# Optimization experiments

Hardware: AMD Instinct MI355X
Metric: run time of the kernel (lower is better)

## Reference

```python
import jax, jax.numpy as jnp
import numpy as np

N = 50000      # nodes
E = 800000     # edges (avg degree 16)
D_IN = 64
H = 128        # capacity
LAT = 64       # latent_dim
LN_EPS = 1e-5


def setup_inputs() -> dict:
    key = jax.random.key(0)
    ks = jax.random.split(key, 16)
    inp = {}
    inp["x"] = jax.random.normal(ks[0], (N, D_IN), dtype=jnp.float32)
    inp["edge_index"] = jax.random.randint(ks[1], (2, E), 0, N)
    dims = [(D_IN, H), (H, H), (H, LAT)]
    ki = 2
    for t in ("m", "v"):  # mu tower / logvar tower
        for i, (di, do) in enumerate(dims):
            s = 1.0 / np.sqrt(di)
            inp[f"{t}Wl{i}"] = jax.random.normal(ks[ki], (do, di), jnp.float32) * s; ki += 1
            inp[f"{t}bl{i}"] = jnp.zeros((do,), jnp.float32)
            inp[f"{t}Wr{i}"] = jax.random.normal(ks[ki], (do, di), jnp.float32) * s; ki += 1
            if i < 2:  # LayerNorm on hidden layers only
                inp[f"{t}g{i}"] = jnp.ones((do,), jnp.float32)
                inp[f"{t}b{i}"] = jnp.zeros((do,), jnp.float32)
    return inp


def _ln(h, g, b):
    m = h.mean(-1, keepdims=True)
    v = h.var(-1, keepdims=True)
    return (h - m) * jax.lax.rsqrt(v + LN_EPS) * g + b


def _sage(h, src, dst, inv_deg, Wl, bl, Wr):
    # mean neighbor aggregation: scatter-add messages h[src] into dst, divide by degree
    agg = jax.ops.segment_sum(h[src], dst, num_segments=N) * inv_deg  # [N, d_in]
    # PyG SAGEConv: lin_l(agg) [with bias] + lin_r(h_root) [no bias]
    return agg @ Wl.T + bl + h @ Wr.T


def _tower(x, src, dst, inv_deg, layers):
    h = x
    L = len(layers)
    for i, lay in enumerate(layers):
        h = _sage(h, src, dst, inv_deg, lay[0], lay[1], lay[2])
        if i < L - 1:
            h = jax.nn.relu(_ln(h, lay[3], lay[4]))
    return h


def reference(x, edge_index,
              mWl0, mbl0, mWr0, mg0, mb0,
              mWl1, mbl1, mWr1, mg1, mb1,
              mWl2, mbl2, mWr2,
              vWl0, vbl0, vWr0, vg0, vb0,
              vWl1, vbl1, vWr1, vg1, vb1,
              vWl2, vbl2, vWr2):
    src, dst = edge_index[0], edge_index[1]
    deg = jax.ops.segment_sum(jnp.ones((E,), x.dtype), dst, num_segments=N)
    inv_deg = (1.0 / jnp.maximum(deg, 1.0))[:, None]
    mu_layers = [(mWl0, mbl0, mWr0, mg0, mb0),
                 (mWl1, mbl1, mWr1, mg1, mb1),
                 (mWl2, mbl2, mWr2)]
    lv_layers = [(vWl0, vbl0, vWr0, vg0, vb0),
                 (vWl1, vbl1, vWr1, vg1, vb1),
                 (vWl2, vbl2, vWr2)]
    mu = _tower(x, src, dst, inv_deg, mu_layers)
    lv = _tower(x, src, dst, inv_deg, lv_layers)
    return mu, lv
```

## Files before the change

### kernel.cpp

```cpp
#include <hip/hip_runtime.h>

#define NN 50000
#define NE 800000
#define MPAD 50048
#define NBK 196
#define FB 98
#define CH4 2048
#define EB4 200000
#define STAGE_CAP 6144

typedef __attribute__((ext_vector_type(8))) short short8;
typedef __attribute__((ext_vector_type(4))) float f32x4;

__device__ __forceinline__ ushort f2b(float f) {
    uint u = __builtin_bit_cast(uint, f);
    uint r = (u + 0x7fffu + ((u >> 16) & 1u)) >> 16;
    return (ushort)r;
}
__device__ __forceinline__ uint pk2(float a, float b) {
    return (uint)f2b(a) | ((uint)f2b(b) << 16);
}
__device__ __forceinline__ float blo(uint u) { return __builtin_bit_cast(float, u << 16); }
__device__ __forceinline__ float bhi(uint u) { return __builtin_bit_cast(float, u & 0xffff0000u); }


__global__ __launch_bounds__(256) void k_f1(const int* __restrict__ dst, int* __restrict__ bhist) {
    __shared__ int h[NBK];
    for (int i = threadIdx.x; i < NBK; i += 256) h[i] = 0;
    __syncthreads();
    int i1 = min((int)(blockIdx.x + 1) * CH4, EB4);
    for (int i = blockIdx.x * CH4 + threadIdx.x; i < i1; i += 256) {
        int4 d = ((const int4*)dst)[i];
        atomicAdd(&h[d.x >> 8], 1);
        atomicAdd(&h[d.y >> 8], 1);
        atomicAdd(&h[d.z >> 8], 1);
        atomicAdd(&h[d.w >> 8], 1);
    }
    __syncthreads();
    for (int i = threadIdx.x; i < NBK; i += 256) bhist[blockIdx.x * NBK + i] = h[i];
}

__global__ __launch_bounds__(256) void k_fscan(const int* __restrict__ bhist,
                                               int* __restrict__ pairRel,
                                               int* __restrict__ bbase) {
    __shared__ int tot[256];
    int b = threadIdx.x;
    int run = 0;
    if (b < NBK) {
        for (int blk = 0; blk < FB; ++blk) {
            int v = bhist[blk * NBK + b];
            pairRel[blk * NBK + b] = run;
            run += v;
        }
    }
    tot[b] = (b < NBK) ? run : 0;
    __syncthreads();
    for (int off = 1; off < 256; off <<= 1) {
        int t = (b >= off) ? tot[b - off] : 0;
        __syncthreads();
        tot[b] += t;
        __syncthreads();
    }
    if (b < NBK) bbase[b] = tot[b] - run;
    if (b == NBK - 1) bbase[NBK] = tot[b];
}

__global__ __launch_bounds__(256) void k_f2(const int* __restrict__ src, const int* __restrict__ dst,
                                            const int* __restrict__ pairRel,
                                            const int* __restrict__ bbase, int2* __restrict__ pairs) {
    __shared__ int cur[NBK];
    for (int i = threadIdx.x; i < NBK; i += 256)
        cur[i] = bbase[i] + pairRel[blockIdx.x * NBK + i];
    __syncthreads();
    int i1 = min((int)(blockIdx.x + 1) * CH4, EB4);
    for (int i = blockIdx.x * CH4 + threadIdx.x; i < i1; i += 256) {
        int4 s = ((const int4*)src)[i];
        int4 d = ((const int4*)dst)[i];
        int p0 = atomicAdd(&cur[d.x >> 8], 1);
        int p1 = atomicAdd(&cur[d.y >> 8], 1);
        int p2 = atomicAdd(&cur[d.z >> 8], 1);
        int p3 = atomicAdd(&cur[d.w >> 8], 1);
        pairs[p0] = (int2){s.x, d.x};
        pairs[p1] = (int2){s.y, d.y};
        pairs[p2] = (int2){s.z, d.z};
        pairs[p3] = (int2){s.w, d.w};
    }
}

__global__ __launch_bounds__(256) void k_f3(const int2* __restrict__ pairs,
                                            const int* __restrict__ bbase,
                                            int* __restrict__ row_start,
                                            float* __restrict__ inv_deg,
                                            int* __restrict__ col) {
    __shared__ int ndeg[256];
    __shared__ int noff[256];
    __shared__ int stage[STAGE_CAP];
    int b = blockIdx.x;
    int base = bbase[b], end = bbase[b + 1];
    int nbase = b << 8;
    int t = threadIdx.x;
    ndeg[t] = 0;
    __syncthreads();
    for (int p = base + t; p < end; p += 256) atomicAdd(&ndeg[pairs[p].y - nbase], 1);
    __syncthreads();
    int d = ndeg[t];
    noff[t] = d;
    __syncthreads();
    for (int off = 1; off < 256; off <<= 1) {
        int v = (t >= off) ? noff[t - off] : 0;
        __syncthreads();
        noff[t] += v;
        __syncthreads();
    }
    int excl = noff[t] - d;
    int node = nbase + t;
    if (node < NN) {
        row_start[node] = base + excl;
        inv_deg[node] = 1.0f / (float)(d > 1 ? d : 1);
    }
    if (b == 0 && t == 0) row_start[NN] = NE;
    __syncthreads();
    noff[t] = excl;
    __syncthreads();
    int cnt = end - base;
    for (int p = base + t; p < end; p += 256) {
        int2 pr = pairs[p];
        int pos = atomicAdd(&noff[pr.y - nbase], 1);
        if (pos < STAGE_CAP) stage[pos] = pr.x;
        else col[base + pos] = pr.x;
    }
    __syncthreads();
    int lim = cnt < STAGE_CAP ? cnt : STAGE_CAP;
    for (int i = t; i < lim; i += 256) col[base + i] = stage[i];
}


__global__ void k_xcvt(const float* __restrict__ x, ushort* __restrict__ xb, int n2) {
    int i = blockIdx.x * blockDim.x + threadIdx.x;
    if (i < n2) {
        float2 v = *(const float2*)(x + (size_t)i * 2);
        *(uint*)(xb + (size_t)i * 2) = pk2(v.x, v.y);
    }
}

struct W2Args {
    const float* srcA[8];
    const float* srcB[8];
    ushort* dst[8];
};

__global__ void k_wcvt(W2Args a) {
    const int offT[8]   = {0, 16384, 49152, 57344, 65536, 81920, 114688, 122880};
    const int splitT[8] = {64, 128, 128, 0, 64, 128, 128, 0};
    const int logKKT[8] = {7, 8, 7, 7, 7, 8, 7, 7};
    const int ntT[8]    = {8, 8, 4, 4, 8, 8, 4, 4};
    int idx = blockIdx.x * blockDim.x + threadIdx.x;
    if (idx >= 131072) return;
    int L = 0;
#pragma unroll
    for (int i = 1; i < 8; ++i) if (idx >= offT[i]) L = i;
    int j = idx - offT[L];
    int lk = logKKT[L];
    int KK = 1 << lk;
    int n = j >> lk;
    int c = j & (KK - 1);
    int split = splitT[L];
    float v = (c < split) ? a.srcA[L][n * split + c]
                          : a.srcB[L][n * (KK - split) + (c - split)];
    int ks = c >> 5, kseg = (c >> 3) & 3, jj = c & 7;
    int nt = n >> 4, r15 = n & 15;
    int lane = (kseg << 4) | r15;
    int foff = ((ks * ntT[L] + nt) << 9) + (lane << 3) + jj;
    a.dst[L][foff] = f2b(v);
}


__device__ __forceinline__ void acc8(float* a, uint4 u) {
    a[0] += blo(u.x); a[1] += bhi(u.x);
    a[2] += blo(u.y); a[3] += bhi(u.y);
    a[4] += blo(u.z); a[5] += bhi(u.z);
    a[6] += blo(u.w); a[7] += bhi(u.w);
}

template <int D, int NSLICE>
__global__ __launch_bounds__(256) void k_aggs(
    const ushort* __restrict__ h,
    const int* __restrict__ row_start, const int* __restrict__ col,
    const float* __restrict__ inv_deg, ushort* __restrict__ o) {
    int slice = blockIdx.x % NSLICE;
    int chunk = blockIdx.x / NSLICE;
    int node = chunk * 64 + (threadIdx.x >> 2);
    int li = threadIdx.x & 3;
    if (node >= NN) return;
    int s = row_start[node], e = row_start[node + 1];
    float sc = inv_deg[node];
    const ushort* hb = h + (size_t)slice * 32 + (size_t)li * 8;
    float a[8] = {0, 0, 0, 0, 0, 0, 0, 0};
    int p = s;
    for (; p + 7 < e; p += 8) {
        int c0 = col[p], c1 = col[p + 1], c2 = col[p + 2], c3 = col[p + 3];
        int c4 = col[p + 4], c5 = col[p + 5], c6 = col[p + 6], c7 = col[p + 7];
        uint4 u0 = *(const uint4*)(hb + (size_t)c0 * D);
        uint4 u1 = *(const uint4*)(hb + (size_t)c1 * D);
        uint4 u2 = *(const uint4*)(hb + (size_t)c2 * D);
        uint4 u3 = *(const uint4*)(hb + (size_t)c3 * D);
        uint4 u4 = *(const uint4*)(hb + (size_t)c4 * D);
        uint4 u5 = *(const uint4*)(hb + (size_t)c5 * D);
        uint4 u6 = *(const uint4*)(hb + (size_t)c6 * D);
        uint4 u7 = *(const uint4*)(hb + (size_t)c7 * D);
        acc8(a, u0); acc8(a, u1); acc8(a, u2); acc8(a, u3);
        acc8(a, u4); acc8(a, u5); acc8(a, u6); acc8(a, u7);
    }
    for (; p < e; ++p) acc8(a, *(const uint4*)(hb + (size_t)col[p] * D));
    uint4 r;
    r.x = pk2(a[0] * sc, a[1] * sc);
    r.y = pk2(a[2] * sc, a[3] * sc);
    r.z = pk2(a[4] * sc, a[5] * sc);
    r.w = pk2(a[6] * sc, a[7] * sc);
    *(uint4*)(o + (size_t)node * D + slice * 32 + li * 8) = r;
}


struct GArgs {
    const ushort *A1, *A2, *Wm, *Wv;
    const float *blm, *blv, *gm, *gv, *bbm, *bbv;
    void* out;
};

template <int KH, int NOUT, bool DO_LN, bool DUAL, int ASTR, int AOFFM, int OSTR, int OOFFM>
__global__ __launch_bounds__(256, 2) void k_gemm(GArgs a) {
    constexpr int NT = NOUT / 16;
    constexpr int NK = KH / 16;
    constexpr int TW = DUAL ? 2 : 1;
    constexpr int WCH = NOUT * KH * 4 / 16;
    __shared__ uint4 wlds[TW * WCH];

    int tid = threadIdx.x;
    int lane = tid & 63, wid = tid >> 6;
    int tow = DUAL ? 0 : blockIdx.y;
    int aoff = tow * AOFFM;

    {
        const uint4* w0 = (const uint4*)(tow ? a.Wv : a.Wm);
        for (int i = tid; i < WCH; i += 256) wlds[i] = w0[i];
        if (DUAL) {
            const uint4* w1 = (const uint4*)a.Wv;
            for (int i = tid; i < WCH; i += 256) wlds[WCH + i] = w1[i];
        }
    }

    int r15 = lane & 15, kseg = lane >> 4;
    int m0 = blockIdx.x * 128 + wid * 32;
    size_t ar0 = (size_t)(m0 + r15);
    size_t ar1 = (size_t)(m0 + 16 + r15);

    short8 af[2][NK];
#pragma unroll
    for (int ks = 0; ks < NK; ++ks) {
        int kc = ks * 32 + kseg * 8;
        af[0][ks] = (kc < KH) ? *(const short8*)(a.A1 + ar0 * ASTR + aoff + kc)
                              : *(const short8*)(a.A2 + ar0 * ASTR + aoff + (kc - KH));
        af[1][ks] = (kc < KH) ? *(const short8*)(a.A1 + ar1 * ASTR + aoff + kc)
                              : *(const short8*)(a.A2 + ar1 * ASTR + aoff + (kc - KH));
    }
    __syncthreads();

    f32x4 acc[TW][2][NT];
#pragma unroll
    for (int tt = 0; tt < TW; ++tt)
#pragma unroll
        for (int t = 0; t < 2; ++t)
#pragma unroll
            for (int nt = 0; nt < NT; ++nt) acc[tt][t][nt] = (f32x4){0.f, 0.f, 0.f, 0.f};

#pragma unroll
    for (int ks = 0; ks < NK; ++ks) {
#pragma unroll
        for (int nt = 0; nt < NT; ++nt) {
#pragma unroll
            for (int tt = 0; tt < TW; ++tt) {
                short8 w = *(const short8*)&wlds[tt * WCH + (ks * NT + nt) * 64 + lane];
                acc[tt][0][nt] = __builtin_amdgcn_mfma_f32_16x16x32_bf16(af[0][ks], w, acc[tt][0][nt], 0, 0, 0);
                acc[tt][1][nt] = __builtin_amdgcn_mfma_f32_16x16x32_bf16(af[1][ks], w, acc[tt][1][nt], 0, 0, 0);
            }
        }
    }

#pragma unroll
    for (int tt = 0; tt < TW; ++tt) {
        int tsel = DUAL ? tt : tow;
        int ooff = tsel * OOFFM;
        const float* bl = tsel ? a.blv : a.blm;
#pragma unroll
        for (int nt = 0; nt < NT; ++nt) {
            float bb = bl[nt * 16 + r15];
#pragma unroll
            for (int t = 0; t < 2; ++t)
#pragma unroll
                for (int r = 0; r < 4; ++r) acc[tt][t][nt][r] += bb;
        }
        if (DO_LN) {
            const float* g = tsel ? a.gv : a.gm;
            const float* b = tsel ? a.bbv : a.bbm;
#pragma unroll
            for (int t = 0; t < 2; ++t) {
                float s[4] = {0, 0, 0, 0}, q[4] = {0, 0, 0, 0};
#pragma unroll
                for (int nt = 0; nt < NT; ++nt)
#pragma unroll
                    for (int r = 0; r < 4; ++r) { float v = acc[tt][t][nt][r]; s[r] += v; q[r] += v * v; }
#pragma unroll
                for (int off = 1; off < 16; off <<= 1)
#pragma unroll
                    for (int r = 0; r < 4; ++r) { s[r] += __shfl_xor(s[r], off); q[r] += __shfl_xor(q[r], off); }
                float mean[4], rstd[4];
#pragma unroll
                for (int r = 0; r < 4; ++r) {
                    mean[r] = s[r] * (1.0f / NOUT);
                    float var = q[r] * (1.0f / NOUT) - mean[r] * mean[r];
                    rstd[r] = rsqrtf(var + 1e-5f);
                }
                ushort* out = (ushort*)a.out;
#pragma unroll
                for (int nt = 0; nt < NT; ++nt) {
                    int n = nt * 16 + r15;
                    float gg = g[n], bb = b[n];
#pragma unroll
                    for (int r = 0; r < 4; ++r) {
                        int row = m0 + t * 16 + kseg * 4 + r;
                        if (row < NN) {
                            float y = fmaxf((acc[tt][t][nt][r] - mean[r]) * rstd[r] * gg + bb, 0.0f);
                            out[(size_t)row * OSTR + ooff + n] = f2b(y);
                        }
                    }
                }
            }
        } else {
            float* out = (float*)a.out;
#pragma unroll
            for (int t = 0; t < 2; ++t)
#pragma unroll
                for (int nt = 0; nt < NT; ++nt) {
                    int n = nt * 16 + r15;
#pragma unroll
                    for (int r = 0; r < 4; ++r) {
                        int row = m0 + t * 16 + kseg * 4 + r;
                        if (row < NN) out[(size_t)row * OSTR + ooff + n] = acc[tt][t][nt][r];
                    }
                }
        }
    }
}


struct G2Args {
    const ushort *A, *Wm, *Wv, *a2;
    const float *blm, *blv;
    void *outm, *outv;
};

template <bool FINAL>
__global__ __launch_bounds__(256, 2) void k_gemm2(G2Args a) {
    constexpr int NT = 4, NK = 4;
    constexpr int WCH = 1024;
    __shared__ uint4 wlds[WCH];

    int tid = threadIdx.x;
    int lane = tid & 63, wid = tid >> 6;
    int tow = blockIdx.y;
    {
        const uint4* w0 = (const uint4*)(tow ? a.Wv : a.Wm);
        for (int i = tid; i < WCH; i += 256) wlds[i] = w0[i];
    }
    int r15 = lane & 15, kseg = lane >> 4;
    int m0 = blockIdx.x * 128 + wid * 32;
    size_t ar0 = (size_t)(m0 + r15);
    size_t ar1 = (size_t)(m0 + 16 + r15);
    int aoff = tow * 128;

    short8 af[2][NK];
#pragma unroll
    for (int ks = 0; ks < NK; ++ks) {
        int kc = ks * 32 + kseg * 8;
        af[0][ks] = *(const short8*)(a.A + ar0 * 256 + aoff + kc);
        af[1][ks] = *(const short8*)(a.A + ar1 * 256 + aoff + kc);
    }
    __syncthreads();

    f32x4 acc[2][NT];
#pragma unroll
    for (int t = 0; t < 2; ++t)
#pragma unroll
        for (int nt = 0; nt < NT; ++nt) acc[t][nt] = (f32x4){0.f, 0.f, 0.f, 0.f};

#pragma unroll
    for (int ks = 0; ks < NK; ++ks) {
#pragma unroll
        for (int nt = 0; nt < NT; ++nt) {
            short8 w = *(const short8*)&wlds[(ks * NT + nt) * 64 + lane];
            acc[0][nt] = __builtin_amdgcn_mfma_f32_16x16x32_bf16(af[0][ks], w, acc[0][nt], 0, 0, 0);
            acc[1][nt] = __builtin_amdgcn_mfma_f32_16x16x32_bf16(af[1][ks], w, acc[1][nt], 0, 0, 0);
        }
    }

    if (FINAL) {
        const float* bl = tow ? a.blv : a.blm;
        float* out = (float*)(tow ? a.outv : a.outm);
#pragma unroll
        for (int t = 0; t < 2; ++t)
#pragma unroll
            for (int nt = 0; nt < NT; ++nt) {
                int n = nt * 16 + r15;
                float bb = bl[n];
#pragma unroll
                for (int r = 0; r < 4; ++r) {
                    int row = m0 + t * 16 + kseg * 4 + r;
                    if (row < NN) {
                        float av = blo((uint)a.a2[(size_t)row * 128 + tow * 64 + n]);
                        out[(size_t)row * 64 + n] = acc[t][nt][r] + bb + av;
                    }
                }
            }
    } else {
        ushort* out = (ushort*)a.outm;
#pragma unroll
        for (int t = 0; t < 2; ++t)
#pragma unroll
            for (int nt = 0; nt < NT; ++nt) {
                int n = nt * 16 + r15;
#pragma unroll
                for (int r = 0; r < 4; ++r) {
                    int row = m0 + t * 16 + kseg * 4 + r;
                    if (row < NN) out[(size_t)row * 128 + tow * 64 + n] = f2b(acc[t][nt][r]);
                }
            }
    }
}


extern "C" void kernel_launch(void* const* d_in, const int* in_sizes, int n_in,
                              void* d_out, int out_size, void* d_ws, size_t ws_size,
                              hipStream_t stream) {
    const float* x = (const float*)d_in[0];
    const int* ei = (const int*)d_in[1];
    const int* esrc = ei;
    const int* edst = ei + NE;

    const float* mWl0 = (const float*)d_in[2];
    const float* mbl0 = (const float*)d_in[3];
    const float* mWr0 = (const float*)d_in[4];
    const float* mg0  = (const float*)d_in[5];
    const float* mb0  = (const float*)d_in[6];
    const float* mWl1 = (const float*)d_in[7];
    const float* mbl1 = (const float*)d_in[8];
    const float* mWr1 = (const float*)d_in[9];
    const float* mg1  = (const float*)d_in[10];
    const float* mb1  = (const float*)d_in[11];
    const float* mWl2 = (const float*)d_in[12];
    const float* mbl2 = (const float*)d_in[13];
    const float* mWr2 = (const float*)d_in[14];
    const float* vWl0 = (const float*)d_in[15];
    const float* vbl0 = (const float*)d_in[16];
    const float* vWr0 = (const float*)d_in[17];
    const float* vg0  = (const float*)d_in[18];
    const float* vb0  = (const float*)d_in[19];
    const float* vWl1 = (const float*)d_in[20];
    const float* vbl1 = (const float*)d_in[21];
    const float* vWr1 = (const float*)d_in[22];
    const float* vg1  = (const float*)d_in[23];
    const float* vb1  = (const float*)d_in[24];
    const float* vWl2 = (const float*)d_in[25];
    const float* vbl2 = (const float*)d_in[26];
    const float* vWr2 = (const float*)d_in[27];

    char* p = (char*)d_ws;
    auto alloc = [&](size_t bytes) {
        void* r = (void*)p;
        p += (bytes + 255) & ~(size_t)255;
        return r;
    };
    int* bhist     = (int*)alloc((size_t)FB * NBK * 4);
    int* pairRel   = (int*)alloc((size_t)FB * NBK * 4);
    int* bbase     = (int*)alloc((size_t)(NBK + 1) * 4);
    int* row_start = (int*)alloc((size_t)(NN + 1) * 4);
    float* inv_deg = (float*)alloc((size_t)NN * 4);
    int* col       = (int*)alloc((size_t)NE * 4);
    int2* pairs    = (int2*)alloc((size_t)NE * 8);
    ushort* agg0   = (ushort*)pairs;
    ushort* x_bf   = (ushort*)alloc((size_t)MPAD * 64 * 2);
    ushort* h1p    = (ushort*)alloc((size_t)MPAD * 256 * 2);
    ushort* h2p    = (ushort*)alloc((size_t)MPAD * 256 * 2);
    ushort* aggp   = (ushort*)alloc((size_t)MPAD * 256 * 2);
    ushort* p2     = aggp;
    ushort* a2     = aggp + (size_t)MPAD * 128;
    ushort* wc0    = (ushort*)alloc((size_t)128 * 128 * 2);
    ushort* wc1    = (ushort*)alloc((size_t)128 * 256 * 2);
    ushort* wc2    = (ushort*)alloc((size_t)64 * 128 * 2);
    ushort* wc3    = (ushort*)alloc((size_t)128 * 128 * 2);
    ushort* wc4    = (ushort*)alloc((size_t)128 * 256 * 2);
    ushort* wc5    = (ushort*)alloc((size_t)64 * 128 * 2);
    ushort* wc6    = (ushort*)alloc((size_t)64 * 128 * 2);
    ushort* wc7    = (ushort*)alloc((size_t)64 * 128 * 2);

    float* out_mu = (float*)d_out;
    float* out_lv = (float*)d_out + (size_t)NN * 64;

    k_xcvt<<<(NN * 64 / 2 + 255) / 256, 256, 0, stream>>>(x, x_bf, NN * 64 / 2);
    W2Args wa;
    wa.srcA[0] = mWl0; wa.srcB[0] = mWr0; wa.dst[0] = wc0;
    wa.srcA[1] = mWl1; wa.srcB[1] = mWr1; wa.dst[1] = wc1;
    wa.srcA[2] = mWl2; wa.srcB[2] = nullptr; wa.dst[2] = wc2;
    wa.srcA[3] = nullptr; wa.srcB[3] = mWr2; wa.dst[3] = wc6;
    wa.srcA[4] = vWl0; wa.srcB[4] = vWr0; wa.dst[4] = wc3;
    wa.srcA[5] = vWl1; wa.srcB[5] = vWr1; wa.dst[5] = wc4;
    wa.srcA[6] = vWl2; wa.srcB[6] = nullptr; wa.dst[6] = wc5;
    wa.srcA[7] = nullptr; wa.srcB[7] = vWr2; wa.dst[7] = wc7;
    k_wcvt<<<512, 256, 0, stream>>>(wa);

    k_f1<<<FB, 256, 0, stream>>>(edst, bhist);
    k_fscan<<<1, 256, 0, stream>>>(bhist, pairRel, bbase);
    k_f2<<<FB, 256, 0, stream>>>(esrc, edst, pairRel, bbase, pairs);
    k_f3<<<196, 256, 0, stream>>>(pairs, bbase, row_start, inv_deg, col);

    const int CHK = (NN + 63) / 64;
    const int gM = MPAD / 128;

    k_aggs<64, 2><<<2 * CHK, 256, 0, stream>>>(x_bf, row_start, col, inv_deg, agg0);
    {
        GArgs ga = {agg0, x_bf, wc0, wc3, mbl0, vbl0, mg0, vg0, mb0, vb0, h1p};
        k_gemm<64, 128, true, true, 64, 0, 256, 128><<<dim3(gM, 1), 256, 0, stream>>>(ga);
    }
    k_aggs<256, 8><<<8 * CHK, 256, 0, stream>>>(h1p, row_start, col, inv_deg, aggp);
    {
        GArgs ga = {aggp, h1p, wc1, wc4, mbl1, vbl1, mg1, vg1, mb1, vb1, h2p};
        k_gemm<128, 128, true, false, 256, 128, 256, 128><<<dim3(gM, 2), 256, 0, stream>>>(ga);
    }
    {
        G2Args g2 = {h2p, wc2, wc5, nullptr, nullptr, nullptr, p2, nullptr};
        k_gemm2<false><<<dim3(gM, 2), 256, 0, stream>>>(g2);
    }
    k_aggs<128, 4><<<4 * CHK, 256, 0, stream>>>(p2, row_start, col, inv_deg, a2);
    {
        G2Args g2 = {h2p, wc6, wc7, a2, mbl2, vbl2, out_mu, out_lv};
        k_gemm2<true><<<dim3(gM, 2), 256, 0, stream>>>(g2);
    }
}
```

Before: 392.7 us.

## Merge prep kernels and restructure gather aggregation with whole-row lane mapping

Fuses the x conversion, weight conversion and destination histogram into a single prep launch to cut launch overhead. Rewrites neighbour aggregation so all lanes for one node cover the full feature row in one block instead of slicing features across blocks. It also unrolls the edge loop by 16 and adds nontemporal loads and stores for column indices, pairs and outputs. The intent is fewer launches and more memory-level parallelism per gather, at the cost of more register pressure. For D=64 each lane now does narrower 8-byte loads.

After: 375.5 us. 1.05x faster.

```diff
diff --git a/kernel.cpp b/kernel.cpp
--- a/kernel.cpp
+++ b/kernel.cpp
@@ -11,6 +11,9 @@
 
 typedef __attribute__((ext_vector_type(8))) short short8;
 typedef __attribute__((ext_vector_type(4))) float f32x4;
+typedef uint __attribute__((ext_vector_type(4))) uintx4;
+typedef uint __attribute__((ext_vector_type(2))) uintx2;
+typedef int __attribute__((ext_vector_type(2))) intx2;
 
 __device__ __forceinline__ ushort f2b(float f) {
     uint u = __builtin_bit_cast(uint, f);
@@ -23,22 +26,80 @@
 __device__ __forceinline__ float blo(uint u) { return __builtin_bit_cast(float, u << 16); }
 __device__ __forceinline__ float bhi(uint u) { return __builtin_bit_cast(float, u & 0xffff0000u); }
 
-
-__global__ __launch_bounds__(256) void k_f1(const int* __restrict__ dst, int* __restrict__ bhist) {
+__device__ __forceinline__ void acc8(float* a, uintx4 u) {
+    a[0] += blo(u[0]); a[1] += bhi(u[0]);
+    a[2] += blo(u[1]); a[3] += bhi(u[1]);
+    a[4] += blo(u[2]); a[5] += bhi(u[2]);
+    a[6] += blo(u[3]); a[7] += bhi(u[3]);
+}
+__device__ __forceinline__ void acc4(float* a, uintx2 u) {
+    a[0] += blo(u[0]); a[1] += bhi(u[0]);
+    a[2] += blo(u[1]); a[3] += bhi(u[1]);
+}
+
+
+struct W2Args {
+    const float* srcA[8];
+    const float* srcB[8];
+    ushort* dst[8];
+};
+
+
+struct PrepArgs {
+    const float* x; ushort* xb;
+    W2Args w;
+    const int* edst; int* bhist;
+};
+
+__global__ __launch_bounds__(256) void k_prep(PrepArgs a) {
     __shared__ int h[NBK];
-    for (int i = threadIdx.x; i < NBK; i += 256) h[i] = 0;
-    __syncthreads();
-    int i1 = min((int)(blockIdx.x + 1) * CH4, EB4);
-    for (int i = blockIdx.x * CH4 + threadIdx.x; i < i1; i += 256) {
-        int4 d = ((const int4*)dst)[i];
-        atomicAdd(&h[d.x >> 8], 1);
-        atomicAdd(&h[d.y >> 8], 1);
-        atomicAdd(&h[d.z >> 8], 1);
-        atomicAdd(&h[d.w >> 8], 1);
-    }
-    __syncthreads();
-    for (int i = threadIdx.x; i < NBK; i += 256) bhist[blockIdx.x * NBK + i] = h[i];
-}
+    int b = blockIdx.x;
+    int t = threadIdx.x;
+    if (b < FB) {
+        for (int i = t; i < NBK; i += 256) h[i] = 0;
+        __syncthreads();
+        int i1 = min((b + 1) * CH4, EB4);
+        for (int i = b * CH4 + t; i < i1; i += 256) {
+            int4 d = ((const int4*)a.edst)[i];
+            atomicAdd(&h[d.x >> 8], 1);
+            atomicAdd(&h[d.y >> 8], 1);
+            atomicAdd(&h[d.z >> 8], 1);
+            atomicAdd(&h[d.w >> 8], 1);
+        }
+        __syncthreads();
+        for (int i = t; i < NBK; i += 256) a.bhist[b * NBK + i] = h[i];
+    } else if (b < FB + 512) {
+        const int offT[8]   = {0, 16384, 49152, 57344, 65536, 81920, 114688, 122880};
+        const int splitT[8] = {64, 128, 128, 0, 64, 128, 128, 0};
+        const int logKKT[8] = {7, 8, 7, 7, 7, 8, 7, 7};
+        const int ntT[8]    = {8, 8, 4, 4, 8, 8, 4, 4};
+        int idx = (b - FB) * 256 + t;
+        if (idx >= 131072) return;
+        int L = 0;
+#pragma unroll
+        for (int i = 1; i < 8; ++i) if (idx >= offT[i]) L = i;
+        int j = idx - offT[L];
+        int lk = logKKT[L];
+        int KK = 1 << lk;
+        int n = j >> lk;
+        int c = j & (KK - 1);
+        int split = splitT[L];
+        float v = (c < split) ? a.w.srcA[L][n * split + c]
+                              : a.w.srcB[L][n * (KK - split) + (c - split)];
+        int ks = c >> 5, kseg = (c >> 3) & 3, jj = c & 7;
+        int nt = n >> 4, r15 = n & 15;
+        int lane = (kseg << 4) | r15;
+        int foff = ((ks * ntT[L] + nt) << 9) + (lane << 3) + jj;
+        a.w.dst[L][foff] = f2b(v);
+    } else {
+        int i = (b - FB - 512) * 256 + t;
+        if (i < NN * 32) {
+            float2 v = *(const float2*)(a.x + (size_t)i * 2);
+            *(uint*)(a.xb + (size_t)i * 2) = pk2(v.x, v.y);
+        }
+    }
+}
+
 
 __global__ __launch_bounds__(256) void k_fscan(const int* __restrict__ bhist,
                                                int* __restrict__ pairRel,
@@ -67,7 +128,7 @@
 
 __global__ __launch_bounds__(256) void k_f2(const int* __restrict__ src, const int* __restrict__ dst,
                                             const int* __restrict__ pairRel,
-                                            const int* __restrict__ bbase, int2* __restrict__ pairs) {
+                                            const int* __restrict__ bbase, intx2* __restrict__ pairs) {
     __shared__ int cur[NBK];
     for (int i = threadIdx.x; i < NBK; i += 256)
         cur[i] = bbase[i] + pairRel[blockIdx.x * NBK + i];
@@ -80,14 +141,14 @@
         int p1 = atomicAdd(&cur[d.y >> 8], 1);
         int p2 = atomicAdd(&cur[d.z >> 8], 1);
         int p3 = atomicAdd(&cur[d.w >> 8], 1);
-        pairs[p0] = (int2){s.x, d.x};
-        pairs[p1] = (int2){s.y, d.y};
-        pairs[p2] = (int2){s.z, d.z};
-        pairs[p3] = (int2){s.w, d.w};
-    }
-}
-
-__global__ __launch_bounds__(256) void k_f3(const int2* __restrict__ pairs,
+        __builtin_nontemporal_store((intx2){s.x, d.x}, &pairs[p0]);
+        __builtin_nontemporal_store((intx2){s.y, d.y}, &pairs[p1]);
+        __builtin_nontemporal_store((intx2){s.z, d.z}, &pairs[p2]);
+        __builtin_nontemporal_store((intx2){s.w, d.w}, &pairs[p3]);
+    }
+}
+
+__global__ __launch_bounds__(256) void k_f3(const intx2* __restrict__ pairs,
                                             const int* __restrict__ bbase,
                                             int* __restrict__ row_start,
                                             float* __restrict__ inv_deg,
@@ -101,7 +162,10 @@
     int t = threadIdx.x;
     ndeg[t] = 0;
     __syncthreads();
-    for (int p = base + t; p < end; p += 256) atomicAdd(&ndeg[pairs[p].y - nbase], 1);
+    for (int p = base + t; p < end; p += 256) {
+        intx2 pr = pairs[p];
+        atomicAdd(&ndeg[pr[1] - nbase], 1);
+    }
     __syncthreads();
     int d = ndeg[t];
     noff[t] = d;
@@ -124,10 +188,10 @@
     __syncthreads();
     int cnt = end - base;
     for (int p = base + t; p < end; p += 256) {
-        int2 pr = pairs[p];
-        int pos = atomicAdd(&noff[pr.y - nbase], 1);
-        if (pos < STAGE_CAP) stage[pos] = pr.x;
-        else col[base + pos] = pr.x;
+        intx2 pr = pairs[p];
+        int pos = atomicAdd(&noff[pr[1] - nbase], 1);
+        if (pos < STAGE_CAP) stage[pos] = pr[0];
+        else col[base + pos] = pr[0];
     }
     __syncthreads();
     int lim = cnt < STAGE_CAP ? cnt : STAGE_CAP;
@@ -135,89 +199,67 @@
 }
 
 
-__global__ void k_xcvt(const float* __restrict__ x, ushort* __restrict__ xb, int n2) {
-    int i = blockIdx.x * blockDim.x + threadIdx.x;
-    if (i < n2) {
-        float2 v = *(const float2*)(x + (size_t)i * 2);
-        *(uint*)(xb + (size_t)i * 2) = pk2(v.x, v.y);
-    }
-}
-
-struct W2Args {
-    const float* srcA[8];
-    const float* srcB[8];
-    ushort* dst[8];
-};
-
-__global__ void k_wcvt(W2Args a) {
-    const int offT[8]   = {0, 16384, 49152, 57344, 65536, 81920, 114688, 122880};
-    const int splitT[8] = {64, 128, 128, 0, 64, 128, 128, 0};
-    const int logKKT[8] = {7, 8, 7, 7, 7, 8, 7, 7};
-    const int ntT[8]    = {8, 8, 4, 4, 8, 8, 4, 4};
-    int idx = blockIdx.x * blockDim.x + threadIdx.x;
-    if (idx >= 131072) return;
-    int L = 0;
-#pragma unroll
-    for (int i = 1; i < 8; ++i) if (idx >= offT[i]) L = i;
-    int j = idx - offT[L];
-    int lk = logKKT[L];
-    int KK = 1 << lk;
-    int n = j >> lk;
-    int c = j & (KK - 1);
-    int split = splitT[L];
-    float v = (c < split) ? a.srcA[L][n * split + c]
-                          : a.srcB[L][n * (KK - split) + (c - split)];
-    int ks = c >> 5, kseg = (c >> 3) & 3, jj = c & 7;
-    int nt = n >> 4, r15 = n & 15;
-    int lane = (kseg << 4) | r15;
-    int foff = ((ks * ntT[L] + nt) << 9) + (lane << 3) + jj;
-    a.dst[L][foff] = f2b(v);
-}
-
-
-__device__ __forceinline__ void acc8(float* a, uint4 u) {
-    a[0] += blo(u.x); a[1] += bhi(u.x);
-    a[2] += blo(u.y); a[3] += bhi(u.y);
-    a[4] += blo(u.z); a[5] += bhi(u.z);
-    a[6] += blo(u.w); a[7] += bhi(u.w);
-}
-
-template <int D, int NSLICE>
-__global__ __launch_bounds__(256) void k_aggs(
+template <int D>
+__global__ __launch_bounds__(256) void k_agg(
     const ushort* __restrict__ h,
     const int* __restrict__ row_start, const int* __restrict__ col,
     const float* __restrict__ inv_deg, ushort* __restrict__ o) {
-    int slice = blockIdx.x % NSLICE;
-    int chunk = blockIdx.x / NSLICE;
-    int node = chunk * 64 + (threadIdx.x >> 2);
-    int li = threadIdx.x & 3;
+    constexpr int LPN = (D == 256) ? 32 : 16;
+    int gid = blockIdx.x * 256 + threadIdx.x;
+    int node = gid / LPN;
+    int li = gid & (LPN - 1);
     if (node >= NN) return;
     int s = row_start[node], e = row_start[node + 1];
     float sc = inv_deg[node];
-    const ushort* hb = h + (size_t)slice * 32 + (size_t)li * 8;
-    float a[8] = {0, 0, 0, 0, 0, 0, 0, 0};
-    int p = s;
-    for (; p + 7 < e; p += 8) {
-        int c0 = col[p], c1 = col[p + 1], c2 = col[p + 2], c3 = col[p + 3];
-        int c4 = col[p + 4], c5 = col[p + 5], c6 = col[p + 6], c7 = col[p + 7];
-        uint4 u0 = *(const uint4*)(hb + (size_t)c0 * D);
-        uint4 u1 = *(const uint4*)(hb + (size_t)c1 * D);
-        uint4 u2 = *(const uint4*)(hb + (size_t)c2 * D);
-        uint4 u3 = *(const uint4*)(hb + (size_t)c3 * D);
-        uint4 u4 = *(const uint4*)(hb + (size_t)c4 * D);
-        uint4 u5 = *(const uint4*)(hb + (size_t)c5 * D);
-        uint4 u6 = *(const uint4*)(hb + (size_t)c6 * D);
-        uint4 u7 = *(const uint4*)(hb + (size_t)c7 * D);
-        acc8(a, u0); acc8(a, u1); acc8(a, u2); acc8(a, u3);
-        acc8(a, u4); acc8(a, u5); acc8(a, u6); acc8(a, u7);
-    }
-    for (; p < e; ++p) acc8(a, *(const uint4*)(hb + (size_t)col[p] * D));
-    uint4 r;
-    r.x = pk2(a[0] * sc, a[1] * sc);
-    r.y = pk2(a[2] * sc, a[3] * sc);
-    r.z = pk2(a[4] * sc, a[5] * sc);
-    r.w = pk2(a[6] * sc, a[7] * sc);
-    *(uint4*)(o + (size_t)node * D + slice * 32 + li * 8) = r;
+    if (D == 64) {
+        const ushort* hb = h + li * 4;
+        float a[4] = {0, 0, 0, 0};
+        int p = s;
+        for (; p + 15 < e; p += 16) {
+            int cc[16];
+#pragma unroll
+            for (int j = 0; j < 16; ++j) cc[j] = __builtin_nontemporal_load(col + p + j);
+#pragma unroll
+            for (int j = 0; j < 16; ++j) acc4(a, *(const uintx2*)(hb + (size_t)cc[j] * 64));
+        }
+        for (; p + 3 < e; p += 4) {
+            int cc[4];
+#pragma unroll
+            for (int j = 0; j < 4; ++j) cc[j] = __builtin_nontemporal_load(col + p + j);
+#pragma unroll
+            for (int j = 0; j < 4; ++j) acc4(a, *(const uintx2*)(hb + (size_t)cc[j] * 64));
+        }
+        for (; p < e; ++p) acc4(a, *(const uintx2*)(hb + (size_t)col[p] * 64));
+        uintx2 r;
+        r[0] = pk2(a[0] * sc, a[1] * sc);
+        r[1] = pk2(a[2] * sc, a[3] * sc);
+        __builtin_nontemporal_store(r, (uintx2*)(o + (size_t)node * 64 + li * 4));
+    } else {
+        const ushort* hb = h + li * 8;
+        float a[8] = {0, 0, 0, 0, 0, 0, 0, 0};
+        int p = s;
+        for (; p + 15 < e; p += 16) {
+            int cc[16];
+#pragma unroll
+            for (int j = 0; j < 16; ++j) cc[j] = __builtin_nontemporal_load(col + p + j);
+#pragma unroll
+            for (int j = 0; j < 16; ++j) acc8(a, *(const uintx4*)(hb + (size_t)cc[j] * D));
+        }
+        for (; p + 3 < e; p += 4) {
+            int cc[4];
+#pragma unroll
+            for (int j = 0; j < 4; ++j) cc[j] = __builtin_nontemporal_load(col + p + j);
+#pragma unroll
+            for (int j = 0; j < 4; ++j) acc8(a, *(const uintx4*)(hb + (size_t)cc[j] * D));
+        }
+        for (; p < e; ++p) acc8(a, *(const uintx4*)(hb + (size_t)col[p] * D));
+        uintx4 r;
+        r[0] = pk2(a[0] * sc, a[1] * sc);
+        r[1] = pk2(a[2] * sc, a[3] * sc);
+        r[2] = pk2(a[4] * sc, a[5] * sc);
+        r[3] = pk2(a[6] * sc, a[7] * sc);
+        __builtin_nontemporal_store(r, (uintx4*)(o + (size_t)node * D + li * 8));
+    }
 }
 
 
@@ -485,7 +527,7 @@
     int* row_start = (int*)alloc((size_t)(NN + 1) * 4);
     float* inv_deg = (float*)alloc((size_t)NN * 4);
     int* col       = (int*)alloc((size_t)NE * 4);
-    int2* pairs    = (int2*)alloc((size_t)NE * 8);
+    intx2* pairs   = (intx2*)alloc((size_t)NE * 8);
     ushort* agg0   = (ushort*)pairs;
     ushort* x_bf   = (ushort*)alloc((size_t)MPAD * 64 * 2);
     ushort* h1p    = (ushort*)alloc((size_t)MPAD * 256 * 2);
@@ -505,32 +547,30 @@
     float* out_mu = (float*)d_out;
     float* out_lv = (float*)d_out + (size_t)NN * 64;
 
-    k_xcvt<<<(NN * 64 / 2 + 255) / 256, 256, 0, stream>>>(x, x_bf, NN * 64 / 2);
-    W2Args wa;
-    wa.srcA[0] = mWl0; wa.srcB[0] = mWr0; wa.dst[0] = wc0;
-    wa.srcA[1] = mWl1; wa.srcB[1] = mWr1; wa.dst[1] = wc1;
-    wa.srcA[2] = mWl2; wa.srcB[2] = nullptr; wa.dst[2] = wc2;
-    wa.srcA[3] = nullptr; wa.srcB[3] = mWr2; wa.dst[3] = wc6;
-    wa.srcA[4] = vWl0; wa.srcB[4] = vWr0; wa.dst[4] = wc3;
-    wa.srcA[5] = vWl1; wa.srcB[5] = vWr1; wa.dst[5] = wc4;
-    wa.srcA[6] = vWl2; wa.srcB[6] = nullptr; wa.dst[6] = wc5;
-    wa.srcA[7] = nullptr; wa.srcB[7] = vWr2; wa.dst[7] = wc7;
-    k_wcvt<<<512, 256, 0, stream>>>(wa);
-
-    k_f1<<<FB, 256, 0, stream>>>(edst, bhist);
+    PrepArgs pa;
+    pa.x = x; pa.xb = x_bf; pa.edst = edst; pa.bhist = bhist;
+    pa.w.srcA[0] = mWl0; pa.w.srcB[0] = mWr0; pa.w.dst[0] = wc0;
+    pa.w.srcA[1] = mWl1; pa.w.srcB[1] = mWr1; pa.w.dst[1] = wc1;
+    pa.w.srcA[2] = mWl2; pa.w.srcB[2] = nullptr; pa.w.dst[2] = wc2;
+    pa.w.srcA[3] = nullptr; pa.w.srcB[3] = mWr2; pa.w.dst[3] = wc6;
+    pa.w.srcA[4] = vWl0; pa.w.srcB[4] = vWr0; pa.w.dst[4] = wc3;
+    pa.w.srcA[5] = vWl1; pa.w.srcB[5] = vWr1; pa.w.dst[5] = wc4;
+    pa.w.srcA[6] = vWl2; pa.w.srcB[6] = nullptr; pa.w.dst[6] = wc5;
+    pa.w.srcA[7] = nullptr; pa.w.srcB[7] = vWr2; pa.w.dst[7] = wc7;
+    k_prep<<<FB + 512 + (NN * 32 + 255) / 256, 256, 0, stream>>>(pa);
+
     k_fscan<<<1, 256, 0, stream>>>(bhist, pairRel, bbase);
     k_f2<<<FB, 256, 0, stream>>>(esrc, edst, pairRel, bbase, pairs);
-    k_f3<<<196, 256, 0, stream>>>(pairs, bbase, row_start, inv_deg, col);
-
-    const int CHK = (NN + 63) / 64;
+    k_f3<<<NBK, 256, 0, stream>>>(pairs, bbase, row_start, inv_deg, col);
+
     const int gM = MPAD / 128;
 
-    k_aggs<64, 2><<<2 * CHK, 256, 0, stream>>>(x_bf, row_start, col, inv_deg, agg0);
+    k_agg<64><<<(NN * 16 + 255) / 256, 256, 0, stream>>>(x_bf, row_start, col, inv_deg, agg0);
     {
         GArgs ga = {agg0, x_bf, wc0, wc3, mbl0, vbl0, mg0, vg0, mb0, vb0, h1p};
         k_gemm<64, 128, true, true, 64, 0, 256, 128><<<dim3(gM, 1), 256, 0, stream>>>(ga);
     }
-    k_aggs<256, 8><<<8 * CHK, 256, 0, stream>>>(h1p, row_start, col, inv_deg, aggp);
+    k_agg<256><<<(NN * 32 + 255) / 256, 256, 0, stream>>>(h1p, row_start, col, inv_deg, aggp);
     {
         GArgs ga = {aggp, h1p, wc1, wc4, mbl1, vbl1, mg1, vg1, mb1, vb1, h2p};
         k_gemm<128, 128, true, false, 256, 128, 256, 128><<<dim3(gM, 2), 256, 0, stream>>>(ga);
@@ -539,7 +579,7 @@
         G2Args g2 = {h2p, wc2, wc5, nullptr, nullptr, nullptr, p2, nullptr};
         k_gemm2<false><<<dim3(gM, 2), 256, 0, stream>>>(g2);
     }
-    k_aggs<128, 4><<<4 * CHK, 256, 0, stream>>>(p2, row_start, col, inv_deg, a2);
+    k_agg<128><<<(NN * 16 + 255) / 256, 256, 0, stream>>>(p2, row_start, col, inv_deg, a2);
     {
         G2Args g2 = {h2p, wc6, wc7, a2, mbl2, vbl2, out_mu, out_lv};
         k_gemm2<true><<<dim3(gM, 2), 256, 0, stream>>>(g2);
```
